# Performance work log

Measured on AMD Instinct MI355X. Metric: run time of the kernel, lower is better.

## Reference

```python
import jax, jax.numpy as jnp
import numpy as np

T = 4096
V = 88   # visible_dim
H = 512  # hidden_dim
R = 512  # rnn_hidden_dim
REG_FACTOR = 0.2
GIBBS_STEPS = 20
EPS = 1e-6


def setup_inputs() -> dict:
    key = jax.random.key(0)
    ks = jax.random.split(key, 8)
    scale = 1.0 / np.sqrt(H)
    return {
        "visible": (jax.random.uniform(ks[0], (T, V)) < 0.5).astype(jnp.float32),
        "rand_h": jax.random.uniform(ks[1], (T - 1, GIBBS_STEPS, H), dtype=jnp.float32),
        "rand_v": jax.random.uniform(ks[2], (T - 1, GIBBS_STEPS, V), dtype=jnp.float32),
        "w": jax.random.normal(ks[3], (H, V), dtype=jnp.float32) * scale,
        "wuu": jax.random.normal(ks[4], (R, R), dtype=jnp.float32) * scale,
        "wuv": jax.random.normal(ks[5], (V, R), dtype=jnp.float32) * scale,
        "wuh": jax.random.normal(ks[6], (H, R), dtype=jnp.float32) * scale,
        "wvu": jax.random.normal(ks[7], (R, V), dtype=jnp.float32) * scale,
        "bv": jnp.zeros((V,), jnp.float32),
        "bh": jnp.zeros((H,), jnp.float32),
        "bu": jnp.zeros((R,), jnp.float32),
        "u0": jnp.zeros((R,), jnp.float32),
    }


def reference(visible, rand_h, rand_v, w, wuu, wuv, wuh, wvu, bv, bh, bu, u0):
    time_steps = visible.shape[0]
    v_seq = visible[1:]  # v_t for t = 1..T-1, shape [T-1, V]

    # RNN state depends only on data, not on Gibbs samples -> single scan.
    def u_step(u_prev, v_t):
        u_new = jnp.tanh(wvu @ v_t + wuu @ u_prev + bu)
        return u_new, u_prev  # emit u_{t-1} (bias conditioning state)

    _, u_prev = jax.lax.scan(u_step, u0, v_seq)  # [T-1, R]

    # Per-timestep RBM biases (F.linear(u, W, b) = u @ W.T + b).
    bh_t = u_prev @ wuh.T + bh  # [T-1, H]
    bv_t = u_prev @ wuv.T + bv  # [T-1, V]

    # 20 Gibbs steps, batched over all time steps at once.
    def gibbs_step(v, rands):
        rh, rv = rands  # [T-1, H], [T-1, V]
        p_h = jax.nn.sigmoid(v @ w.T + bh_t)
        h = jax.nn.relu(jnp.sign(p_h - rh))         # Bernoulli sample
        p_v = jax.nn.sigmoid(h @ w + bv_t)
        v_new = jax.nn.relu(jnp.sign(p_v - rv))
        return v_new, None

    neg, _ = jax.lax.scan(
        gibbs_step, v_seq,
        (jnp.swapaxes(rand_h, 0, 1), jnp.swapaxes(rand_v, 0, 1)),
    )  # negative samples [T-1, V]

    # Cross-entropy between data and sigmoid(bv_t), summed then /time_steps.
    y_t = jax.nn.sigmoid(bv_t)
    total_cost = jnp.sum(
        -v_seq * jnp.log(EPS + y_t) - (1.0 - v_seq) * jnp.log(EPS + 1.0 - y_t)
    ) / time_steps

    reg_term = (jnp.linalg.norm(wuv) + jnp.linalg.norm(wuh)) * REG_FACTOR
    total_cost = total_cost + reg_term

    mse = jnp.mean(jnp.abs(v_seq - neg), axis=1)  # per-timestep, [T-1]
    return total_cost, mse, reg_term
```

## Files before the change

kernel.cpp:

```cpp
#include <hip/hip_runtime.h>
#include <cstdint>
#include <cstddef>

#define T4096 4096
#define TM1 4095
#define NV 88
#define NH 512
#define NR 512
#define GS 20
#define EPSV 1e-6f

#define U_OFF 0
#define AB_OFF 2096640
#define BV_OFF 4193280
#define SC_OFF 4553640

__device__ __forceinline__ unsigned int agent_load_u32(const unsigned int* p) {
  return __hip_atomic_load(p, __ATOMIC_RELAXED, __HIP_MEMORY_SCOPE_AGENT);
}
__device__ __forceinline__ void agent_store_f32(float* p, float v) {
  __hip_atomic_store(p, v, __ATOMIC_RELAXED, __HIP_MEMORY_SCOPE_AGENT);
}
__device__ __forceinline__ float sigmoidf_(float x) {
  return 1.0f / (1.0f + expf(-x));
}

__device__ __forceinline__ void store_sc0(float* p, float v) {
  asm volatile("global_store_dword %0, %1, off sc0" :: "v"(p), "v"(v) : "memory");
}
__device__ __forceinline__ unsigned load_sc0(const unsigned* p) {
  unsigned r;
  asm volatile("global_load_dword %0, %1, off sc0\n\ts_waitcnt vmcnt(0)"
               : "=v"(r) : "v"(p) : "memory");
  return r;
}

__device__ __forceinline__ unsigned poll_roll_sc0(const unsigned* p) {
  unsigned rA, r0, r1, r2, r3;
  asm volatile(
    "s_waitcnt vmcnt(0)\n\t"
    "v_mov_b32 %0, -1\n\t"
    "global_load_dword %1, %5, off sc0\n\t"
    "global_load_dword %2, %5, off sc0\n\t"
    "global_load_dword %3, %5, off sc0\n\t"
    "global_load_dword %4, %5, off sc0\n\t"
    "Lr%=:\n\t"
    "s_waitcnt vmcnt(3)\n\t"
    "v_cmp_ne_u32 vcc, -1, %1\n\t"
    "v_cndmask_b32 %0, %0, %1, vcc\n\t"
    "v_cmp_eq_u32 vcc, -1, %0\n\t"
    "s_cbranch_vccz Le%=\n\t"
    "global_load_dword %1, %5, off sc0\n\t"
    "s_waitcnt vmcnt(3)\n\t"
    "v_cmp_ne_u32 vcc, -1, %2\n\t"
    "v_cndmask_b32 %0, %0, %2, vcc\n\t"
    "v_cmp_eq_u32 vcc, -1, %0\n\t"
    "s_cbranch_vccz Le%=\n\t"
    "global_load_dword %2, %5, off sc0\n\t"
    "s_waitcnt vmcnt(3)\n\t"
    "v_cmp_ne_u32 vcc, -1, %3\n\t"
    "v_cndmask_b32 %0, %0, %3, vcc\n\t"
    "v_cmp_eq_u32 vcc, -1, %0\n\t"
    "s_cbranch_vccz Le%=\n\t"
    "global_load_dword %3, %5, off sc0\n\t"
    "s_waitcnt vmcnt(3)\n\t"
    "v_cmp_ne_u32 vcc, -1, %4\n\t"
    "v_cndmask_b32 %0, %0, %4, vcc\n\t"
    "v_cmp_eq_u32 vcc, -1, %0\n\t"
    "s_cbranch_vccz Le%=\n\t"
    "global_load_dword %4, %5, off sc0\n\t"
    "s_branch Lr%=\n\t"
    "Le%=:\n\t"
    "s_waitcnt vmcnt(0)\n\t"
    : "=&v"(rA), "=&v"(r0), "=&v"(r1), "=&v"(r2), "=&v"(r3)
    : "v"(p) : "vcc", "memory");
  return rA;
}
__device__ __forceinline__ unsigned poll_roll_sys(const unsigned* p) {
  unsigned rA, r0, r1, r2, r3;
  asm volatile(
    "s_waitcnt vmcnt(0)\n\t"
    "v_mov_b32 %0, -1\n\t"
    "global_load_dword %1, %5, off sc0 sc1\n\t"
    "global_load_dword %2, %5, off sc0 sc1\n\t"
    "global_load_dword %3, %5, off sc0 sc1\n\t"
    "global_load_dword %4, %5, off sc0 sc1\n\t"
    "Lq%=:\n\t"
    "s_waitcnt vmcnt(3)\n\t"
    "v_cmp_ne_u32 vcc, -1, %1\n\t"
    "v_cndmask_b32 %0, %0, %1, vcc\n\t"
    "v_cmp_eq_u32 vcc, -1, %0\n\t"
    "s_cbranch_vccz Lf%=\n\t"
    "global_load_dword %1, %5, off sc0 sc1\n\t"
    "s_waitcnt vmcnt(3)\n\t"
    "v_cmp_ne_u32 vcc, -1, %2\n\t"
    "v_cndmask_b32 %0, %0, %2, vcc\n\t"
    "v_cmp_eq_u32 vcc, -1, %0\n\t"
    "s_cbranch_vccz Lf%=\n\t"
    "global_load_dword %2, %5, off sc0 sc1\n\t"
    "s_waitcnt vmcnt(3)\n\t"
    "v_cmp_ne_u32 vcc, -1, %3\n\t"
    "v_cndmask_b32 %0, %0, %3, vcc\n\t"
    "v_cmp_eq_u32 vcc, -1, %0\n\t"
    "s_cbranch_vccz Lf%=\n\t"
    "global_load_dword %3, %5, off sc0 sc1\n\t"
    "s_waitcnt vmcnt(3)\n\t"
    "v_cmp_ne_u32 vcc, -1, %4\n\t"
    "v_cndmask_b32 %0, %0, %4, vcc\n\t"
    "v_cmp_eq_u32 vcc, -1, %0\n\t"
    "s_cbranch_vccz Lf%=\n\t"
    "global_load_dword %4, %5, off sc0 sc1\n\t"
    "s_branch Lq%=\n\t"
    "Lf%=:\n\t"
    "s_waitcnt vmcnt(0)\n\t"
    : "=&v"(rA), "=&v"(r0), "=&v"(r1), "=&v"(r2), "=&v"(r3)
    : "v"(p) : "vcc", "memory");
  return rA;
}

__global__ __launch_bounds__(256) void k_a(const float* __restrict__ visible,
                                           const float* __restrict__ wvu,
                                           const float* __restrict__ bu,
                                           float* __restrict__ A) {
  __shared__ float vbuf[NV * 8];
  const int tid = threadIdx.x;
  const int t0 = blockIdx.x * 8;
  for (int idx = tid; idx < NV * 8; idx += 256) {
    int j = idx / NV, v = idx - j * NV;
    int t = t0 + j;
    vbuf[v * 8 + j] = (t < TM1) ? visible[(size_t)(t + 1) * NV + v] : 0.f;
  }
  __syncthreads();
  for (int rr = 0; rr < 2; rr++) {
    int r = tid + rr * 256;
    float b0 = bu[r];
    float acc[8];
#pragma unroll
    for (int j = 0; j < 8; j++) acc[j] = b0;
    const float* wr = wvu + (size_t)r * NV;
    for (int v = 0; v < NV; v++) {
      float wv = wr[v];
#pragma unroll
      for (int j = 0; j < 8; j++) acc[j] = fmaf(wv, vbuf[v * 8 + j], acc[j]);
    }
#pragma unroll
    for (int j = 0; j < 8; j++) {
      int t = t0 + j;
      if (t < TM1) A[(size_t)t * NR + r] = acc[j];
    }
  }
}

__global__ __launch_bounds__(256) void k_r(const float* __restrict__ wuv,
                                           const float* __restrict__ wuh,
                                           float* __restrict__ sc) {
  size_t stride = (size_t)gridDim.x * 256;
  size_t gid = (size_t)blockIdx.x * 256 + threadIdx.x;
  float s1 = 0.f, s2 = 0.f;
  for (size_t i = gid; i < (size_t)NV * NR; i += stride) { float x = wuv[i]; s1 = fmaf(x, x, s1); }
  for (size_t i = gid; i < (size_t)NH * NR; i += stride) { float x = wuh[i]; s2 = fmaf(x, x, s2); }
  for (int off = 32; off > 0; off >>= 1) {
    s1 += __shfl_down(s1, off, 64);
    s2 += __shfl_down(s2, off, 64);
  }
  if ((threadIdx.x & 63) == 0) {
    atomicAdd(&sc[1], s1);
    atomicAdd(&sc[2], s2);
  }
}

__global__ __launch_bounds__(512, 2) void k_u7(const float* __restrict__ wuu,
                                               const float* __restrict__ A,
                                               const float* __restrict__ u0,
                                               float* __restrict__ U,
                                               unsigned* __restrict__ ub) {
  __shared__ int s_slot;
  __shared__ int s_fast;
  __shared__ float u_lds[NR];
  __shared__ float partials[1024];
  const int tid = threadIdx.x;
  unsigned* claimc = ub + 8;
  unsigned* winner = ub + 16;
  unsigned* hs     = ub + 17;
  unsigned* vd     = ub + 33;

  if (tid == 0) {
    unsigned xcd;
    asm volatile("s_getreg_b32 %0, hwreg(HW_REG_XCC_ID, 0, 4)" : "=s"(xcd));
    xcd &= 7u;
    unsigned c = atomicAdd(&claimc[xcd], 1u);
    int slot = -1;
    if (c < 4u) {
      if (c == 3u) atomicCAS(winner, 0xFFFFFFFFu, xcd);
      unsigned wnr;
      do { wnr = agent_load_u32(winner); } while (wnr == 0xFFFFFFFFu);
      if (wnr == xcd) slot = (int)c;
    }
    s_slot = slot;
  }
  __syncthreads();
  const int slot = s_slot;
  if (slot < 0) return;

  if (tid == 0) {
    int fast = 1;
    for (int round = 0; round < 4 && fast; ++round) {
      unsigned* hw = hs + round * 4;
      store_sc0((float*)&hw[slot], 0.0f);
      for (int o = 0; o < 4; ++o) {
        if (o == slot) continue;
        int ok = 0;
        for (int it = 0; it < 300; ++it) {
          if (load_sc0(&hw[o]) != 0xFFFFFFFFu) { ok = 1; break; }
        }
        if (!ok) fast = 0;
      }
    }
    __hip_atomic_store(&vd[slot], (unsigned)(fast ? 1 : 0),
                       __ATOMIC_RELAXED, __HIP_MEMORY_SCOPE_AGENT);
    for (int o = 0; o < 4; ++o) {
      unsigned v;
      do { v = agent_load_u32(&vd[o]); } while (v == 0xFFFFFFFFu);
      if (v != 1u) fast = 0;
    }
    s_fast = fast;
  }
  __syncthreads();
  const int fast = s_fast;

  const int lane = tid & 63;
  const int kc   = tid >> 6;
  const int r0   = slot * 128;
  const int rA   = lane;
  const int rB   = lane + 64;

  float WregA[64], WregB[64];
  {
    const float* wra = wuu + (size_t)(r0 + rA) * NR + kc * 64;
    const float* wrb = wuu + (size_t)(r0 + rB) * NR + kc * 64;
#pragma unroll
    for (int i = 0; i < 16; i++) {
      ((float4*)WregA)[i] = ((const float4*)wra)[i];
      ((float4*)WregB)[i] = ((const float4*)wrb)[i];
    }
  }
#pragma unroll
  for (int i = 0; i < 64; i++) asm volatile("" : "+v"(WregA[i]));
#pragma unroll
  for (int i = 0; i < 64; i++) asm volatile("" : "+v"(WregB[i]));

  if (tid < NR) u_lds[tid] = u0[tid];
  if (tid < 128) agent_store_f32(&U[r0 + tid], u0[r0 + tid]);
  float a_cur = (tid < 128) ? A[r0 + tid] : 0.f;
  int pword = -1;
  if (tid >= 128 && tid < 512) {
    int p = tid - 128;
    pword = (p < r0) ? p : p + 128;
  }
  __syncthreads();

  for (int t = 1; t <= TM1 - 1; t++) {
    float acc0 = 0.f, acc1 = 0.f;
    const float* uc = u_lds + kc * 64;
#pragma unroll
    for (int i = 0; i < 64; i += 4) {
      float4 uv = *(const float4*)(uc + i);
      acc0 = fmaf(WregA[i],     uv.x, acc0);
      acc1 = fmaf(WregB[i],     uv.x, acc1);
      acc0 = fmaf(WregA[i + 1], uv.y, acc0);
      acc1 = fmaf(WregB[i + 1], uv.y, acc1);
      acc0 = fmaf(WregA[i + 2], uv.z, acc0);
      acc1 = fmaf(WregB[i + 2], uv.z, acc1);
      acc0 = fmaf(WregA[i + 3], uv.w, acc0);
      acc1 = fmaf(WregB[i + 3], uv.w, acc1);
    }
    partials[kc * 128 + rA] = acc0;
    partials[kc * 128 + rB] = acc1;
    __syncthreads();
    if (tid < 128) {
      float s = a_cur;
#pragma unroll
      for (int kk = 0; kk < 8; kk++) s += partials[kk * 128 + tid];
      float val = tanhf(s);
      if (fast) store_sc0(&U[(size_t)t * NR + r0 + tid], val);
      else      agent_store_f32(&U[(size_t)t * NR + r0 + tid], val);
      u_lds[r0 + tid] = val;
      a_cur = A[(size_t)t * NR + r0 + tid];
    } else if (pword >= 0) {
      const unsigned* p = (const unsigned*)(U + (size_t)t * NR) + pword;
      unsigned w = fast ? poll_roll_sc0(p) : poll_roll_sys(p);
      u_lds[pword] = __uint_as_float(w);
    }
    __syncthreads();
  }
}

__global__ __launch_bounds__(256) void k_bh(const float* __restrict__ Uu,
                                            const float* __restrict__ wuh,
                                            const float* __restrict__ wuv,
                                            const float* __restrict__ bh,
                                            const float* __restrict__ bv,
                                            const float* __restrict__ visible,
                                            float* __restrict__ bht,
                                            float* __restrict__ bvt,
                                            float* __restrict__ sc) {
  __shared__ float uT[NR * 20];
  __shared__ float red[256];
  const int tid = threadIdx.x;
  const int t0 = blockIdx.x * 16;
  const int nt = min(16, TM1 - t0);
  for (int idx = tid; idx < 16 * NR; idx += 256) {
    int tt = idx >> 9, k = idx & 511;
    uT[k * 20 + tt] = (tt < nt) ? Uu[(size_t)(t0 + tt) * NR + k] : 0.f;
  }
  __syncthreads();
  const int h1 = tid, h2 = tid + 256;
  const bool hasv = tid < NV;
  float acc1[16], acc2[16], accv[16];
#pragma unroll
  for (int i = 0; i < 16; i++) acc1[i] = acc2[i] = accv[i] = 0.f;
  const float* w1p = wuh + (size_t)h1 * NR;
  const float* w2p = wuh + (size_t)h2 * NR;
  const float* wvp = wuv + (size_t)(hasv ? tid : 0) * NR;
  for (int k = 0; k < NR; k++) {
    float u16[16];
#pragma unroll
    for (int q = 0; q < 4; q++) *(float4*)(u16 + 4 * q) = *(const float4*)(uT + k * 20 + 4 * q);
    float a = w1p[k], b = w2p[k];
    float c = hasv ? wvp[k] : 0.f;
#pragma unroll
    for (int i = 0; i < 16; i++) {
      acc1[i] = fmaf(a, u16[i], acc1[i]);
      acc2[i] = fmaf(b, u16[i], acc2[i]);
      accv[i] = fmaf(c, u16[i], accv[i]);
    }
  }
  float bh1 = bh[h1], bh2 = bh[h2];
#pragma unroll
  for (int i = 0; i < 16; i++) {
    if (i < nt) {
      bht[(size_t)(t0 + i) * NH + h1] = acc1[i] + bh1;
      bht[(size_t)(t0 + i) * NH + h2] = acc2[i] + bh2;
    }
  }
  float ce = 0.f;
  if (hasv) {
    float bvv = bv[tid];
    for (int i = 0; i < nt; i++) {
      float x = accv[i] + bvv;
      bvt[(size_t)(t0 + i) * NV + tid] = x;
      float y = sigmoidf_(x);
      float vs = visible[(size_t)(t0 + i + 1) * NV + tid];
      ce += -vs * logf(EPSV + y) - (1.f - vs) * logf(EPSV + 1.f - y);
    }
  }
  red[tid] = ce;
  __syncthreads();
  for (int s = 128; s > 0; s >>= 1) {
    if (tid < s) red[tid] += red[tid + s];
    __syncthreads();
  }
  if (tid == 0) atomicAdd(&sc[0], red[0]);
}

__global__ __launch_bounds__(256) void k_g(const float* __restrict__ w,
                                           const float* __restrict__ visible,
                                           const float* __restrict__ rand_h,
                                           const float* __restrict__ rand_v,
                                           const float* __restrict__ bht,
                                           const float* __restrict__ bvt,
                                           float* __restrict__ out) {
  __shared__ float vlds[NV * 20];
  __shared__ float hlds[NH * 20];
  const int tid = threadIdx.x;
  const int t0 = blockIdx.x * 16;
  const int nt = min(16, TM1 - t0);
  for (int idx = tid; idx < NV * 16; idx += 256) {
    int j = idx / NV, v = idx - j * NV;
    vlds[v * 20 + j] = (j < nt) ? visible[(size_t)(t0 + j + 1) * NV + v] : 0.f;
  }
  for (int idx = tid; idx < NH * 20; idx += 256) hlds[idx] = 0.f;
  __syncthreads();
  const int h1 = tid, h2 = tid + 256;
  const int tg = tid >> 5, vg = tid & 31;
  const int v0 = vg * 4;
  const bool bact = vg < 22;
  for (int k = 0; k < GS; k++) {
    {
      float acc1[16], acc2[16];
#pragma unroll
      for (int i = 0; i < 16; i++) acc1[i] = acc2[i] = 0.f;
      const float* w1p = w + (size_t)h1 * NV;
      const float* w2p = w + (size_t)h2 * NV;
      for (int v = 0; v < NV; v++) {
        float vv[16];
#pragma unroll
        for (int q = 0; q < 4; q++) *(float4*)(vv + 4 * q) = *(const float4*)(vlds + v * 20 + 4 * q);
        float a = w1p[v], b = w2p[v];
#pragma unroll
        for (int i = 0; i < 16; i++) {
          acc1[i] = fmaf(a, vv[i], acc1[i]);
          acc2[i] = fmaf(b, vv[i], acc2[i]);
        }
      }
#pragma unroll
      for (int i = 0; i < 16; i++) {
        if (i < nt) {
          size_t t = (size_t)(t0 + i);
          float x1 = acc1[i] + bht[t * NH + h1];
          float x2 = acc2[i] + bht[t * NH + h2];
          float p1 = sigmoidf_(x1);
          float p2 = sigmoidf_(x2);
          float r1 = rand_h[(t * GS + k) * NH + h1];
          float r2 = rand_h[(t * GS + k) * NH + h2];
          hlds[h1 * 20 + i] = (p1 > r1) ? 1.f : 0.f;
          hlds[h2 * 20 + i] = (p2 > r2) ? 1.f : 0.f;
        }
      }
    }
    __syncthreads();
    if (bact) {
      float acc[2][4];
#pragma unroll
      for (int a = 0; a < 2; a++)
#pragma unroll
        for (int b = 0; b < 4; b++) acc[a][b] = 0.f;
#pragma unroll 4
      for (int h = 0; h < NH; h++) {
        float2 hv = *(const float2*)(hlds + h * 20 + tg * 2);
        float4 w4 = *(const float4*)(w + (size_t)h * NV + v0);
        acc[0][0] = fmaf(hv.x, w4.x, acc[0][0]);
        acc[0][1] = fmaf(hv.x, w4.y, acc[0][1]);
        acc[0][2] = fmaf(hv.x, w4.z, acc[0][2]);
        acc[0][3] = fmaf(hv.x, w4.w, acc[0][3]);
        acc[1][0] = fmaf(hv.y, w4.x, acc[1][0]);
        acc[1][1] = fmaf(hv.y, w4.y, acc[1][1]);
        acc[1][2] = fmaf(hv.y, w4.z, acc[1][2]);
        acc[1][3] = fmaf(hv.y, w4.w, acc[1][3]);
      }
#pragma unroll
      for (int a = 0; a < 2; a++) {
        int tt = tg * 2 + a;
        if (tt < nt) {
          size_t t = (size_t)(t0 + tt);
#pragma unroll
          for (int i = 0; i < 4; i++) {
            int v = v0 + i;
            float x = acc[a][i] + bvt[t * NV + v];
            float p = sigmoidf_(x);
            float r = rand_v[(t * GS + k) * NV + v];
            vlds[v * 20 + tt] = (p > r) ? 1.f : 0.f;
          }
        }
      }
    }
    __syncthreads();
  }
  if (tid < 16 && tid < nt) {
    int tt = tid;
    float s = 0.f;
    for (int v = 0; v < NV; v++) {
      float vs = visible[(size_t)(t0 + tt + 1) * NV + v];
      s += fabsf(vs - vlds[v * 20 + tt]);
    }
    out[1 + t0 + tt] = s / 88.f;
  }
}

__global__ void k_f(const float* __restrict__ sc, float* __restrict__ out) {
  float reg = 0.2f * (sqrtf(sc[1]) + sqrtf(sc[2]));
  out[0] = sc[0] / 4096.f + reg;
  out[4096] = reg;
}

extern "C" void kernel_launch(void* const* d_in, const int* in_sizes, int n_in,
                              void* d_out, int out_size, void* d_ws, size_t ws_size,
                              hipStream_t stream) {
  const float* visible = (const float*)d_in[0];
  const float* rand_h  = (const float*)d_in[1];
  const float* rand_v  = (const float*)d_in[2];
  const float* w       = (const float*)d_in[3];
  const float* wuu     = (const float*)d_in[4];
  const float* wuv     = (const float*)d_in[5];
  const float* wuh     = (const float*)d_in[6];
  const float* wvu     = (const float*)d_in[7];
  const float* bv      = (const float*)d_in[8];
  const float* bh      = (const float*)d_in[9];
  const float* bu      = (const float*)d_in[10];
  const float* u0      = (const float*)d_in[11];
  float* out = (float*)d_out;
  float* ws = (float*)d_ws;

  float* Uarr = ws + U_OFF;
  float* Aarr = ws + AB_OFF;
  float* bht  = ws + AB_OFF;
  float* bvt  = ws + BV_OFF;
  float* sc   = ws + SC_OFF;
  unsigned* ub = (unsigned*)sc;

  hipMemsetAsync(Uarr, 0xFF, (size_t)TM1 * NR * sizeof(float), stream);
  hipMemsetAsync(sc, 0, 64, stream);
  hipMemsetAsync((char*)sc + 64, 0xFF, 96, stream);

  k_a<<<512, 256, 0, stream>>>(visible, wvu, bu, Aarr);
  k_r<<<64, 256, 0, stream>>>(wuv, wuh, sc);
  k_u7<<<64, 512, 0, stream>>>(wuu, Aarr, u0, Uarr, ub);
  k_bh<<<256, 256, 0, stream>>>(Uarr, wuh, wuv, bh, bv, visible, bht, bvt, sc);
  k_g<<<256, 256, 0, stream>>>(w, visible, rand_h, rand_v, bht, bvt, out);
  k_f<<<1, 1, 0, stream>>>(sc, out);
}
```

Measured before the change: 5.738 ms.

## Remove second barrier per RNN step via wave-private u chunks and double-buffered partials

Restructures the sequential RNN recurrence kernel so each wave owns its own 64-element slice of the hidden state in LDS and fills it itself, either from its own reduction result or by polling the peer block's global output. Double-buffering the partial-sum array lets one __syncthreads per step replace the previous two. The reduction is spread across the two waves whose slice matches this block's rows, so the value they compute feeds straight into their next step. This shortens the critical path of the latency-bound 4094-step loop, at the cost of subtler cross-wave ordering that depends on the double buffer and on wave-local LDS writes being visible within the wave.

```diff
diff --git a/kernel.cpp b/kernel.cpp
--- a/kernel.cpp
+++ b/kernel.cpp
@@ -169,15 +169,15 @@
   }
 }
 
-__global__ __launch_bounds__(512, 2) void k_u7(const float* __restrict__ wuu,
+__global__ __launch_bounds__(512, 2) void k_u8(const float* __restrict__ wuu,
                                                const float* __restrict__ A,
                                                const float* __restrict__ u0,
                                                float* __restrict__ U,
                                                unsigned* __restrict__ ub) {
   __shared__ int s_slot;
   __shared__ int s_fast;
-  __shared__ float u_lds[NR];
-  __shared__ float partials[1024];
+  __shared__ float u_buf[NR];
+  __shared__ float partials[2][1024];
   const int tid = threadIdx.x;
   unsigned* claimc = ub + 8;
   unsigned* winner = ub + 16;
@@ -231,13 +231,14 @@
   const int lane = tid & 63;
   const int kc   = tid >> 6;
   const int r0   = slot * 128;
-  const int rA   = lane;
-  const int rB   = lane + 64;
+  const bool is_red = (kc >> 1) == slot;
+  const int s_row = ((kc & 1) << 6) + lane;
+  float* ubw = u_buf + kc * 64;
 
   float WregA[64], WregB[64];
   {
-    const float* wra = wuu + (size_t)(r0 + rA) * NR + kc * 64;
-    const float* wrb = wuu + (size_t)(r0 + rB) * NR + kc * 64;
+    const float* wra = wuu + (size_t)(r0 + lane) * NR + kc * 64;
+    const float* wrb = wuu + (size_t)(r0 + lane + 64) * NR + kc * 64;
 #pragma unroll
     for (int i = 0; i < 16; i++) {
       ((float4*)WregA)[i] = ((const float4*)wra)[i];
@@ -249,50 +250,56 @@
 #pragma unroll
   for (int i = 0; i < 64; i++) asm volatile("" : "+v"(WregB[i]));
 
-  if (tid < NR) u_lds[tid] = u0[tid];
-  if (tid < 128) agent_store_f32(&U[r0 + tid], u0[r0 + tid]);
-  float a_cur = (tid < 128) ? A[r0 + tid] : 0.f;
-  int pword = -1;
-  if (tid >= 128 && tid < 512) {
-    int p = tid - 128;
-    pword = (p < r0) ? p : p + 128;
-  }
-  __syncthreads();
-
-  for (int t = 1; t <= TM1 - 1; t++) {
-    float acc0 = 0.f, acc1 = 0.f;
-    const float* uc = u_lds + kc * 64;
-#pragma unroll
-    for (int i = 0; i < 64; i += 4) {
-      float4 uv = *(const float4*)(uc + i);
-      acc0 = fmaf(WregA[i],     uv.x, acc0);
-      acc1 = fmaf(WregB[i],     uv.x, acc1);
-      acc0 = fmaf(WregA[i + 1], uv.y, acc0);
-      acc1 = fmaf(WregB[i + 1], uv.y, acc1);
-      acc0 = fmaf(WregA[i + 2], uv.z, acc0);
-      acc1 = fmaf(WregB[i + 2], uv.z, acc1);
-      acc0 = fmaf(WregA[i + 3], uv.w, acc0);
-      acc1 = fmaf(WregB[i + 3], uv.w, acc1);
-    }
-    partials[kc * 128 + rA] = acc0;
-    partials[kc * 128 + rB] = acc1;
-    __syncthreads();
-    if (tid < 128) {
-      float s = a_cur;
-#pragma unroll
-      for (int kk = 0; kk < 8; kk++) s += partials[kk * 128 + tid];
-      float val = tanhf(s);
-      if (fast) store_sc0(&U[(size_t)t * NR + r0 + tid], val);
-      else      agent_store_f32(&U[(size_t)t * NR + r0 + tid], val);
-      u_lds[r0 + tid] = val;
-      a_cur = A[(size_t)t * NR + r0 + tid];
-    } else if (pword >= 0) {
-      const unsigned* p = (const unsigned*)(U + (size_t)t * NR) + pword;
+  float val = 0.f, a_cur = 0.f;
+  if (is_red) {
+    agent_store_f32(&U[r0 + s_row], u0[r0 + s_row]);
+    a_cur = A[r0 + s_row];
+  }
+  __syncthreads();
+
+#define KU_STEP(T_, UVAL_) do {                                                \
+    ubw[lane] = (UVAL_);                                                       \
+    float acc0 = 0.f, acc1 = 0.f;                                              \
+    _Pragma("unroll")                                                          \
+    for (int i = 0; i < 64; i += 4) {                                          \
+      float4 uv = *(const float4*)(ubw + i);                                   \
+      acc0 = fmaf(WregA[i],     uv.x, acc0);                                   \
+      acc1 = fmaf(WregB[i],     uv.x, acc1);                                   \
+      acc0 = fmaf(WregA[i + 1], uv.y, acc0);                                   \
+      acc1 = fmaf(WregB[i + 1], uv.y, acc1);                                   \
+      acc0 = fmaf(WregA[i + 2], uv.z, acc0);                                   \
+      acc1 = fmaf(WregB[i + 2], uv.z, acc1);                                   \
+      acc0 = fmaf(WregA[i + 3], uv.w, acc0);                                   \
+      acc1 = fmaf(WregB[i + 3], uv.w, acc1);                                   \
+    }                                                                          \
+    float* pb = partials[(T_) & 1];                                            \
+    pb[kc * 128 + lane] = acc0;                                                \
+    pb[kc * 128 + lane + 64] = acc1;                                           \
+    __syncthreads();                                                           \
+    if (is_red) {                                                              \
+      float s = a_cur;                                                         \
+      _Pragma("unroll")                                                        \
+      for (int kk = 0; kk < 8; kk++) s += pb[kk * 128 + s_row];                \
+      val = tanhf(s);                                                          \
+      if (fast) store_sc0(&U[(size_t)(T_) * NR + r0 + s_row], val);            \
+      else      agent_store_f32(&U[(size_t)(T_) * NR + r0 + s_row], val);      \
+      a_cur = A[(size_t)(T_) * NR + r0 + s_row];    \
+    }                                                                          \
+  } while (0)
+
+  KU_STEP(1, u0[kc * 64 + lane]);
+  for (int t = 2; t <= TM1 - 1; t++) {
+    float u_val;
+    if (is_red) {
+      u_val = val;
+    } else {
+      const unsigned* p = (const unsigned*)(U + (size_t)(t - 1) * NR) + kc * 64 + lane;
       unsigned w = fast ? poll_roll_sc0(p) : poll_roll_sys(p);
-      u_lds[pword] = __uint_as_float(w);
-    }
-    __syncthreads();
-  }
+      u_val = __uint_as_float(w);
+    }
+    KU_STEP(t, u_val);
+  }
+#undef KU_STEP
 }
 
 __global__ __launch_bounds__(256) void k_bh(const float* __restrict__ Uu,
@@ -504,7 +511,7 @@
 
   k_a<<<512, 256, 0, stream>>>(visible, wvu, bu, Aarr);
   k_r<<<64, 256, 0, stream>>>(wuv, wuh, sc);
-  k_u7<<<64, 512, 0, stream>>>(wuu, Aarr, u0, Uarr, ub);
+  k_u8<<<64, 512, 0, stream>>>(wuu, Aarr, u0, Uarr, ub);
   k_bh<<<256, 256, 0, stream>>>(Uarr, wuh, wuv, bh, bv, visible, bht, bvt, sc);
   k_g<<<256, 256, 0, stream>>>(w, visible, rand_h, rand_v, bht, bvt, out);
   k_f<<<1, 1, 0, stream>>>(sc, out);
```

Result: faster. 5.485 ms (-4.4%).
